# Kernel tuning notes

Hardware: AMD Instinct MI355X
Metric: run time of the kernel (lower is better)

Reference implementation:

```python
import jax, jax.numpy as jnp
import numpy as np

B, N, NODE_DIM = 64, 64, 192
H = 256          # node_hidden_dim
PDIM = 64        # property_embedding_dim
NUM_EDGE_TYPE = 5
T = 4            # message-passing rounds
E = 16384        # total edges (flattened batched graph)
E_SEL = 65536    # selected candidate pairs


def setup_inputs() -> dict:
    key = jax.random.key(0)
    ks = jax.random.split(key, 24)
    def g(k, shape, scale=0.05):
        return jax.random.normal(k, shape, dtype=jnp.float32) * scale
    inp = {
        "x": jax.random.normal(ks[0], (B, N, NODE_DIM), dtype=jnp.float32),
        "edge_index": jax.random.randint(ks[1], (2, E), 0, B * N, dtype=jnp.int32),
        "edge_attr": jax.random.uniform(ks[2], (E, NUM_EDGE_TYPE), dtype=jnp.float32),
        "props": jax.random.normal(ks[3], (B, 1), dtype=jnp.float32),
        "sel_b": jax.random.randint(ks[4], (E_SEL,), 0, B, dtype=jnp.int32),
        "sel_i": jax.random.randint(ks[5], (E_SEL,), 0, N, dtype=jnp.int32),
        "sel_j": jax.random.randint(ks[6], (E_SEL,), 0, N, dtype=jnp.int32),
        "golden_edge": jax.random.randint(ks[7], (E_SEL,), 0, NUM_EDGE_TYPE, dtype=jnp.int32),
        # parameters
        "W_prop": g(ks[8], (1, PDIM)), "b_prop": jnp.zeros((PDIM,), jnp.float32),
        "W_in": g(ks[9], (NODE_DIM, H)), "b_in": jnp.zeros((H,), jnp.float32),
        "W_msg": g(ks[10], (H + NUM_EDGE_TYPE, H)), "b_msg": jnp.zeros((H,), jnp.float32),
        "W_upd": g(ks[11], (2 * H, H)), "b_upd": jnp.zeros((H,), jnp.float32),
        "W_add": g(ks[12], (H + PDIM, H)), "b_add": jnp.zeros((H,), jnp.float32),
        "W1": g(ks[13], (2 * H, H)), "b1": jnp.zeros((H,), jnp.float32),
        "W2": g(ks[14], (H, H)), "b2": jnp.zeros((H,), jnp.float32),
        "W3": g(ks[15], (H, 2 * H)), "b3": jnp.zeros((2 * H,), jnp.float32),
        "W_out": g(ks[16], (2 * H, NUM_EDGE_TYPE)), "b_out": jnp.zeros((NUM_EDGE_TYPE,), jnp.float32),
    }
    return inp


def reference(x, edge_index, edge_attr, props, sel_b, sel_i, sel_j, golden_edge,
              W_prop, b_prop, W_in, b_in, W_msg, b_msg, W_upd, b_upd,
              W_add, b_add, W1, b1, W2, b2, W3, b3, W_out, b_out):
    BN = B * N
    node_x = x.reshape(BN, NODE_DIM)
    src, dst = edge_index[0], edge_index[1]

    # --- GNN node embedding (t rounds of message passing, opaque Encoder.embed_node) ---
    h = jax.nn.relu(node_x @ W_in + b_in)                       # [BN, H]
    for _ in range(T):
        msg_in = jnp.concatenate([h[src], edge_attr], axis=-1)  # [E, H+num_edge_type]
        msg = jax.nn.relu(msg_in @ W_msg + b_msg)               # [E, H]
        agg = jax.ops.segment_sum(msg, dst, num_segments=BN)    # [BN, H]
        h = jax.nn.relu(jnp.concatenate([h, agg], axis=-1) @ W_upd + b_upd)

    node_emb = h.reshape(B, N, H)

    # --- property conditioning + addition linear ---
    prop = props @ W_prop + b_prop                               # [B, PDIM]
    propp = jnp.broadcast_to(prop[:, None, :], (B, N, PDIM))
    node_embg = jnp.concatenate([node_emb, propp], axis=-1) @ W_add + b_add  # [B, N, H]

    # --- gather selected (src, dst) pairs directly (equiv. to repeat_interleave + boolean mask) ---
    flat = node_embg.reshape(BN, H)
    src_e = flat[sel_b * N + sel_i]                              # [E_SEL, H]
    dst_e = flat[sel_b * N + sel_j]                              # [E_SEL, H]
    pair = jnp.concatenate([src_e, dst_e], axis=-1)              # [E_SEL, 2H]

    # --- edge predictor MLP (3 layers, ReLU between) + output linear ---
    h1 = jax.nn.relu(pair @ W1 + b1)
    h2 = jax.nn.relu(h1 @ W2 + b2)
    h3 = h2 @ W3 + b3
    logits = h3 @ W_out + b_out                                  # [E_SEL, num_edge_type]

    # --- cross entropy (mean) ---
    logp = jax.nn.log_softmax(logits, axis=-1)
    loss = -jnp.mean(jnp.take_along_axis(logp, golden_edge[:, None].astype(jnp.int32), axis=-1))
    return loss
```

## Files before the change

### kernel.cpp

```cpp
#include <hip/hip_runtime.h>
#include <math.h>

#define BN 4096
#define N_PER_B 64
#define NE 16384
#define NSEL 65536
#define NET 5
#define PD 64
#define H1STR 260
#define FSTR 264
#define PTILES 2

typedef float f32x4 __attribute__((ext_vector_type(4)));
typedef float f32x16 __attribute__((ext_vector_type(16)));
typedef short short8 __attribute__((ext_vector_type(8)));
typedef short short4v __attribute__((ext_vector_type(4)));

__device__ __forceinline__ unsigned short f2bf(float f) {
    unsigned int u = __builtin_bit_cast(unsigned int, f);
    u += 0x7fff + ((u >> 16) & 1);
    return (unsigned short)(u >> 16);
}
__device__ __forceinline__ float bf_lo(unsigned int u) {
    return __builtin_bit_cast(float, u << 16);
}
__device__ __forceinline__ float bf_hi(unsigned int u) {
    return __builtin_bit_cast(float, u & 0xffff0000u);
}
__device__ __forceinline__ unsigned int pack2(float a, float b) {
    return (unsigned)f2bf(a) | ((unsigned)f2bf(b) << 16);
}
__device__ __forceinline__ short8 ld_frag(const unsigned short* p) {
    const short4v lo = *(const short4v*)(p);
    const short4v hi = *(const short4v*)(p + 4);
    return __builtin_shufflevector(lo, hi, 0, 1, 2, 3, 4, 5, 6, 7);
}
__device__ __forceinline__ unsigned int addrelu2(unsigned int a, unsigned int b, unsigned int c) {
    const float lo = fmaxf(bf_lo(a) + bf_lo(b) + bf_lo(c), 0.f);
    const float hi = fmaxf(bf_hi(a) + bf_hi(b) + bf_hi(c), 0.f);
    return pack2(lo, hi);
}

__global__ __launch_bounds__(256) void k_hist(const int* __restrict__ eidx,
                                              int* __restrict__ deg)
{
    const int e = blockIdx.x * 256 + threadIdx.x;
    atomicAdd(&deg[eidx[NE + e]], 1);
}

__global__ __launch_bounds__(256) void csr_scan(const int* __restrict__ deg,
                                                int* __restrict__ row_start,
                                                int* __restrict__ cursor)
{
    __shared__ int sums[256];
    const int tid = threadIdx.x;
    const int base = tid * 16;
    int local[16];
    int s = 0;
    #pragma unroll
    for (int i = 0; i < 16; ++i) { local[i] = s; s += deg[base + i]; }
    sums[tid] = s;
    __syncthreads();
    for (int off = 1; off < 256; off <<= 1) {
        const int v = sums[tid];
        const int add = (tid >= off) ? sums[tid - off] : 0;
        __syncthreads();
        sums[tid] = v + add;
        __syncthreads();
    }
    const int offset = (tid == 0) ? 0 : sums[tid - 1];
    #pragma unroll
    for (int i = 0; i < 16; ++i) {
        const int v = offset + local[i];
        row_start[base + i] = v;
        cursor[base + i] = v;
    }
    if (tid == 255) row_start[4096] = NE;
}

__global__ __launch_bounds__(256) void csr_scatter(const int* __restrict__ eidx,
                                                   int* __restrict__ cursor,
                                                   int* __restrict__ srcs)
{
    const int e = blockIdx.x * 256 + threadIdx.x;
    const int pos = atomicAdd(&cursor[eidx[NE + e]], 1);
    srcs[pos] = eidx[e] | (e << 12);
}

__global__ __launch_bounds__(256) void k_pre(
    const float* __restrict__ W_in, const float* __restrict__ W_msg,
    const float* __restrict__ W_upd, const float* __restrict__ W_add,
    const float* __restrict__ W1, const float* __restrict__ W2,
    const float* __restrict__ W3, const float* __restrict__ b3,
    const float* __restrict__ W_out, const float* __restrict__ b_out,
    const float* __restrict__ props, const float* __restrict__ W_prop,
    const float* __restrict__ b_prop, const float* __restrict__ b_add,
    const float* __restrict__ b_msg, const float* __restrict__ eattr,
    unsigned short* __restrict__ wbf, unsigned short* __restrict__ WfT,
    float* __restrict__ bfv, float* __restrict__ prop_add,
    unsigned short* __restrict__ ETc, float* __restrict__ out,
    int* __restrict__ deg)
{
    __shared__ __align__(16) char smem[16704];
    const int blk = blockIdx.x;
    const int tid = threadIdx.x;

    if (blk < 16) deg[blk * 256 + tid] = 0;
    if (blk == 0 && tid == 0) out[0] = 0.f;

    if (blk < 128) {
        float (*s)[65] = (float(*)[65])smem;
        const int wsel = blk >> 4;
        const int sub = blk & 15;
        const float* src; unsigned short* dst; int K = 256;
        switch (wsel) {
            case 0: src = W_in;              dst = wbf;                         K = 192; break;
            case 1: src = W_msg;             dst = wbf + 49152;                 break;
            case 2: src = W_upd;             dst = wbf + 49152 + 65536;         break;
            case 3: src = W_upd + 256 * 256; dst = wbf + 49152 + 2 * 65536;     break;
            case 4: src = W_add;             dst = wbf + 49152 + 3 * 65536;     break;
            case 5: src = W1;                dst = wbf + 49152 + 4 * 65536;     break;
            case 6: src = W1 + 256 * 256;    dst = wbf + 49152 + 5 * 65536;     break;
            default: src = W2;               dst = wbf + 49152 + 6 * 65536;     break;
        }
        const int k0 = (sub >> 2) * 64;
        const int n0 = (sub & 3) * 64;
        if (k0 >= K) return;
        const int tn = tid & 63;
        const int tg = tid >> 6;
        #pragma unroll
        for (int i = 0; i < 16; ++i) {
            const int kk = tg * 16 + i;
            s[kk][tn] = src[(size_t)(k0 + kk) * 256 + n0 + tn];
        }
        __syncthreads();
        #pragma unroll
        for (int i = 0; i < 16; ++i) {
            const int nn = tg * 16 + i;
            dst[(size_t)(n0 + nn) * K + k0 + tn] = f2bf(s[tn][nn]);
        }
    } else if (blk < 192) {
        const int b = blk - 128;
        const float pv = props[b];
        float acc = b_add[tid];
        for (int p = 0; p < PD; ++p) {
            const float e = fmaf(pv, W_prop[p], b_prop[p]);
            acc = fmaf(e, W_add[(256 + p) * 256 + tid], acc);
        }
        prop_add[b * 256 + tid] = acc;
    } else if (blk < 449) {
        float* part = (float*)smem;
        const int cb = blk - 192;
        float acc[NET] = {0.f, 0.f, 0.f, 0.f, 0.f};
        #pragma unroll
        for (int rep = 0; rep < 2; ++rep) {
            const int j = rep * 256 + tid;
            const float wv = (cb < 256) ? W3[(size_t)cb * 512 + j] : b3[j];
            #pragma unroll
            for (int t = 0; t < NET; ++t) acc[t] = fmaf(wv, W_out[j * NET + t], acc[t]);
        }
        #pragma unroll
        for (int t = 0; t < NET; ++t)
            for (int off = 32; off >= 1; off >>= 1) acc[t] += __shfl_down(acc[t], off);
        if ((tid & 63) == 0) {
            #pragma unroll
            for (int t = 0; t < NET; ++t) part[(tid >> 6) * NET + t] = acc[t];
        }
        __syncthreads();
        if (tid == 0) {
            float s[NET];
            #pragma unroll
            for (int t = 0; t < NET; ++t)
                s[t] = part[t] + part[NET + t] + part[2 * NET + t] + part[3 * NET + t];
            if (cb < 256) {
                #pragma unroll
                for (int t = 0; t < NET; ++t) WfT[t * 256 + cb] = f2bf(s[t]);
                #pragma unroll
                for (int t = NET; t < 16; ++t) WfT[t * 256 + cb] = 0;
            } else {
                #pragma unroll
                for (int t = 0; t < NET; ++t) bfv[t] = s[t] + b_out[t];
            }
        }
    } else {
        float* ea = (float*)smem;
        const int eb = (blk - 449) * 128;
        if (tid < 160)
            *(float4*)&ea[tid * 4] = *(const float4*)(eattr + (size_t)eb * 5 + tid * 4);
        __syncthreads();
        const float* Wme = W_msg + 256 * 256;
        const float w0 = Wme[0 * 256 + tid];
        const float w1 = Wme[1 * 256 + tid];
        const float w2 = Wme[2 * 256 + tid];
        const float w3 = Wme[3 * 256 + tid];
        const float w4 = Wme[4 * 256 + tid];
        const float bm = b_msg[tid];
        for (int i = 0; i < 128; ++i) {
            const float* a = ea + i * 5;
            float v = bm;
            v = fmaf(a[0], w0, v); v = fmaf(a[1], w1, v); v = fmaf(a[2], w2, v);
            v = fmaf(a[3], w3, v); v = fmaf(a[4], w4, v);
            ETc[(size_t)(eb + i) * 256 + tid] = f2bf(v);
        }
    }
}

__global__ __launch_bounds__(1024) void fstep(
    const float* __restrict__ x, const unsigned short* __restrict__ hbuf,
    const unsigned short* __restrict__ Pin, const unsigned short* __restrict__ ETc,
    const int* __restrict__ row_start, const int* __restrict__ srcs,
    const unsigned short* __restrict__ WaT, const unsigned short* __restrict__ WbT,
    const float* __restrict__ bias1,
    const unsigned short* __restrict__ Wp2T, const float* __restrict__ prop_add,
    const unsigned short* __restrict__ W1aT, const unsigned short* __restrict__ W1bT,
    unsigned short* __restrict__ hout, unsigned short* __restrict__ out1,
    unsigned short* __restrict__ out2, int mode)
{
    __shared__ __align__(16) unsigned short Hg[16 * FSTR];
    __shared__ __align__(16) unsigned short Ag[16 * FSTR];
    __shared__ __align__(16) unsigned short Hs[16 * FSTR];
    __shared__ __align__(16) unsigned short H2s[16 * FSTR];
    const int tid = threadIdx.x;
    const int w = tid >> 6;
    const int lane = tid & 63;
    const int q = lane >> 4;
    const int tx = lane & 15;
    const int m0 = blockIdx.x * 16;
    const int col = w * 16 + tx;

    if (mode != 0) {
        {
            const int r = tid >> 6;
            const int c4 = (tid & 63) * 4;
            *(uint2*)&Hg[r * FSTR + c4] =
                *(const uint2*)(hbuf + (size_t)(m0 + r) * 256 + c4);
        }
        {
            const int node = m0 + w;
            const int beg = row_start[node];
            const int end = row_start[node + 1];
            const int c = lane * 4;
            float a0 = 0.f, a1 = 0.f, a2 = 0.f, a3 = 0.f;
            int idx = beg;
            for (; idx + 3 < end; idx += 4) {
                const int k0 = srcs[idx],     k1 = srcs[idx + 1];
                const int k2 = srcs[idx + 2], k3 = srcs[idx + 3];
                const uint2 p0 = *(const uint2*)(Pin + (size_t)(k0 & 4095) * 256 + c);
                const uint2 p1 = *(const uint2*)(Pin + (size_t)(k1 & 4095) * 256 + c);
                const uint2 p2 = *(const uint2*)(Pin + (size_t)(k2 & 4095) * 256 + c);
                const uint2 p3 = *(const uint2*)(Pin + (size_t)(k3 & 4095) * 256 + c);
                const uint2 e0 = *(const uint2*)(ETc + (size_t)(k0 >> 12) * 256 + c);
                const uint2 e1 = *(const uint2*)(ETc + (size_t)(k1 >> 12) * 256 + c);
                const uint2 e2 = *(const uint2*)(ETc + (size_t)(k2 >> 12) * 256 + c);
                const uint2 e3 = *(const uint2*)(ETc + (size_t)(k3 >> 12) * 256 + c);
                a0 += fmaxf(bf_lo(p0.x) + bf_lo(e0.x), 0.f) + fmaxf(bf_lo(p1.x) + bf_lo(e1.x), 0.f)
                    + fmaxf(bf_lo(p2.x) + bf_lo(e2.x), 0.f) + fmaxf(bf_lo(p3.x) + bf_lo(e3.x), 0.f);
                a1 += fmaxf(bf_hi(p0.x) + bf_hi(e0.x), 0.f) + fmaxf(bf_hi(p1.x) + bf_hi(e1.x), 0.f)
                    + fmaxf(bf_hi(p2.x) + bf_hi(e2.x), 0.f) + fmaxf(bf_hi(p3.x) + bf_hi(e3.x), 0.f);
                a2 += fmaxf(bf_lo(p0.y) + bf_lo(e0.y), 0.f) + fmaxf(bf_lo(p1.y) + bf_lo(e1.y), 0.f)
                    + fmaxf(bf_lo(p2.y) + bf_lo(e2.y), 0.f) + fmaxf(bf_lo(p3.y) + bf_lo(e3.y), 0.f);
                a3 += fmaxf(bf_hi(p0.y) + bf_hi(e0.y), 0.f) + fmaxf(bf_hi(p1.y) + bf_hi(e1.y), 0.f)
                    + fmaxf(bf_hi(p2.y) + bf_hi(e2.y), 0.f) + fmaxf(bf_hi(p3.y) + bf_hi(e3.y), 0.f);
            }
            for (; idx < end; ++idx) {
                const int pk = srcs[idx];
                const uint2 pu = *(const uint2*)(Pin + (size_t)(pk & 4095) * 256 + c);
                const uint2 eu = *(const uint2*)(ETc + (size_t)(pk >> 12) * 256 + c);
                a0 += fmaxf(bf_lo(pu.x) + bf_lo(eu.x), 0.f);
                a1 += fmaxf(bf_hi(pu.x) + bf_hi(eu.x), 0.f);
                a2 += fmaxf(bf_lo(pu.y) + bf_lo(eu.y), 0.f);
                a3 += fmaxf(bf_hi(pu.y) + bf_hi(eu.y), 0.f);
            }
            uint2 o; o.x = pack2(a0, a1); o.y = pack2(a2, a3);
            *(uint2*)&Ag[w * FSTR + c] = o;
        }
        __syncthreads();
    }

    f32x4 acc = (f32x4)0.f;
    if (mode == 0) {
        #pragma unroll
        for (int s = 0; s < 6; ++s) {
            const int k0 = s * 32;
            const float* ap = x + (size_t)(m0 + tx) * 192 + k0 + q * 8;
            const float4 v0 = *(const float4*)ap;
            const float4 v1 = *(const float4*)(ap + 4);
            short8 af;
            af[0] = (short)f2bf(v0.x); af[1] = (short)f2bf(v0.y);
            af[2] = (short)f2bf(v0.z); af[3] = (short)f2bf(v0.w);
            af[4] = (short)f2bf(v1.x); af[5] = (short)f2bf(v1.y);
            af[6] = (short)f2bf(v1.z); af[7] = (short)f2bf(v1.w);
            const short8 bfr = *(const short8*)(WaT + (size_t)col * 192 + k0 + q * 8);
            acc = __builtin_amdgcn_mfma_f32_16x16x32_bf16(af, bfr, acc, 0, 0, 0);
        }
    } else {
        #pragma unroll
        for (int s = 0; s < 8; ++s) {
            const int k0 = s * 32;
            const short8 af = *(const short8*)&Hg[tx * FSTR + k0 + q * 8];
            const short8 bfr = *(const short8*)(WaT + (size_t)col * 256 + k0 + q * 8);
            acc = __builtin_amdgcn_mfma_f32_16x16x32_bf16(af, bfr, acc, 0, 0, 0);
        }
        #pragma unroll
        for (int s = 0; s < 8; ++s) {
            const int k0 = s * 32;
            const short8 af = *(const short8*)&Ag[tx * FSTR + k0 + q * 8];
            const short8 bfr = *(const short8*)(WbT + (size_t)col * 256 + k0 + q * 8);
            acc = __builtin_amdgcn_mfma_f32_16x16x32_bf16(af, bfr, acc, 0, 0, 0);
        }
    }
    {
        const float bv = bias1[col];
        #pragma unroll
        for (int r = 0; r < 4; ++r) {
            const int row = q * 4 + r;
            const unsigned short us = f2bf(fmaxf(acc[r] + bv, 0.f));
            Hs[row * FSTR + col] = us;
            if (mode < 2) hout[(size_t)(m0 + row) * 256 + col] = us;
        }
    }
    __syncthreads();

    acc = (f32x4)0.f;
    #pragma unroll
    for (int s = 0; s < 8; ++s) {
        const int k0 = s * 32;
        const short8 af = *(const short8*)&Hs[tx * FSTR + k0 + q * 8];
        const short8 bfr = *(const short8*)(Wp2T + (size_t)col * 256 + k0 + q * 8);
        acc = __builtin_amdgcn_mfma_f32_16x16x32_bf16(af, bfr, acc, 0, 0, 0);
    }
    if (mode < 2) {
        #pragma unroll
        for (int r = 0; r < 4; ++r)
            out1[(size_t)(m0 + q * 4 + r) * 256 + col] = f2bf(acc[r]);
        return;
    }
    {
        const float pv = prop_add[(m0 >> 6) * 256 + col];
        #pragma unroll
        for (int r = 0; r < 4; ++r)
            H2s[(q * 4 + r) * FSTR + col] = f2bf(acc[r] + pv);
    }
    __syncthreads();

    for (int which = 0; which < 2; ++which) {
        const unsigned short* WT = which ? W1bT : W1aT;
        unsigned short* op = which ? out2 : out1;
        acc = (f32x4)0.f;
        #pragma unroll
        for (int s = 0; s < 8; ++s) {
            const int k0 = s * 32;
            const short8 af = *(const short8*)&H2s[tx * FSTR + k0 + q * 8];
            const short8 bfr = *(const short8*)(WT + (size_t)col * 256 + k0 + q * 8);
            acc = __builtin_amdgcn_mfma_f32_16x16x32_bf16(af, bfr, acc, 0, 0, 0);
        }
        #pragma unroll
        for (int r = 0; r < 4; ++r)
            op[(size_t)(m0 + q * 4 + r) * 256 + col] = f2bf(acc[r]);
    }
}

__global__ __launch_bounds__(512, 2) void pair_k(
    const unsigned short* __restrict__ A1t, const unsigned short* __restrict__ A2t,
    const float* __restrict__ b1, const unsigned short* __restrict__ W2T,
    const float* __restrict__ b2, const unsigned short* __restrict__ WfT,
    const float* __restrict__ bfv,
    const int* __restrict__ sel_b, const int* __restrict__ sel_i,
    const int* __restrict__ sel_j, const int* __restrict__ golden,
    float* __restrict__ out)
{
    __shared__ __align__(16) unsigned short sbuf[64 * H1STR];
    __shared__ __align__(16) unsigned short b1s[256];
    __shared__ float Lg[64 * 8];
    __shared__ int sidx[64 * PTILES], didx[64 * PTILES], gold[64 * PTILES];

    const int tid = threadIdx.x;
    const int w = tid >> 6;
    const int lane = tid & 63;
    const int q = lane >> 4;
    const int tx = lane & 15;
    const int m = lane & 31;
    const int hh = lane >> 5;
    const int e0 = blockIdx.x * 64 * PTILES;

    if (tid < 64 * PTILES) {
        const int e = e0 + tid;
        const int b = sel_b[e];
        sidx[tid] = b * N_PER_B + sel_i[e];
        didx[tid] = b * N_PER_B + sel_j[e];
        gold[tid] = golden[e];
    }
    if (tid < 256) b1s[tid] = f2bf(b1[tid]);

    short8 Breg[16];
    {
        const unsigned short* bb = W2T + (size_t)(w * 32 + m) * 256 + hh * 8;
        #pragma unroll
        for (int s = 0; s < 16; ++s)
            Breg[s] = *(const short8*)(bb + s * 16);
    }
    __syncthreads();

    float total = 0.f;

    for (int t = 0; t < PTILES; ++t) {
        {
            const int hw = tid >> 5;
            #pragma unroll
            for (int j = 0; j < 4; ++j) {
                const int p = j * 16 + hw;
                const unsigned short* r1 = A1t + (size_t)sidx[t * 64 + p] * 256 + m * 8;
                const unsigned short* r2 = A2t + (size_t)didx[t * 64 + p] * 256 + m * 8;
                const uint4 u1 = *(const uint4*)r1;
                const uint4 u2 = *(const uint4*)r2;
                const uint4 ub = *(const uint4*)(b1s + m * 8);
                uint2 lo2, hi2;
                lo2.x = addrelu2(u1.x, u2.x, ub.x);
                lo2.y = addrelu2(u1.y, u2.y, ub.y);
                hi2.x = addrelu2(u1.z, u2.z, ub.z);
                hi2.y = addrelu2(u1.w, u2.w, ub.w);
                unsigned short* dbase = sbuf + p * H1STR + m * 8;
                *(uint2*)(dbase) = lo2;
                *(uint2*)(dbase + 4) = hi2;
            }
        }
        __syncthreads();

        f32x16 acc0 = (f32x16)0.f;
        f32x16 acc1 = (f32x16)0.f;
        {
            const unsigned short* a0row = sbuf + (size_t)m * H1STR + hh * 8;
            const unsigned short* a1row = a0row + 32 * H1STR;
            #pragma unroll
            for (int s = 0; s < 16; ++s) {
                const short8 af0 = ld_frag(a0row + s * 16);
                acc0 = __builtin_amdgcn_mfma_f32_32x32x16_bf16(af0, Breg[s], acc0, 0, 0, 0);
                const short8 af1 = ld_frag(a1row + s * 16);
                acc1 = __builtin_amdgcn_mfma_f32_32x32x16_bf16(af1, Breg[s], acc1, 0, 0, 0);
            }
        }
        __syncthreads();

        {
            const int col = w * 32 + m;
            const float bv = b2[col];
            #pragma unroll
            for (int reg = 0; reg < 16; ++reg) {
                const int prow = (reg & 3) + 8 * (reg >> 2) + 4 * hh;
                sbuf[prow * H1STR + col] = f2bf(fmaxf(acc0[reg] + bv, 0.f));
                sbuf[(32 + prow) * H1STR + col] = f2bf(fmaxf(acc1[reg] + bv, 0.f));
            }
        }
        __syncthreads();

        if (w < 4) {
            f32x4 accL = (f32x4)0.f;
            const unsigned short* a2row = sbuf + (size_t)(w * 16 + tx) * H1STR + q * 8;
            const unsigned short* bWf = WfT + (size_t)tx * 256 + q * 8;
            #pragma unroll
            for (int s = 0; s < 8; ++s) {
                const short8 af = ld_frag(a2row + s * 32);
                const short8 bfr = *(const short8*)(bWf + s * 32);
                accL = __builtin_amdgcn_mfma_f32_16x16x32_bf16(af, bfr, accL, 0, 0, 0);
            }
            if (tx < NET) {
                const float bb = bfv[tx];
                #pragma unroll
                for (int reg = 0; reg < 4; ++reg)
                    Lg[(w * 16 + q * 4 + reg) * 8 + tx] = accL[reg] + bb;
            }
        }
        __syncthreads();

        if (tid < 64) {
            float lg[NET];
            #pragma unroll
            for (int tt = 0; tt < NET; ++tt) lg[tt] = Lg[tid * 8 + tt];
            float mx = lg[0];
            #pragma unroll
            for (int tt = 1; tt < NET; ++tt) mx = fmaxf(mx, lg[tt]);
            float s = 0.f;
            #pragma unroll
            for (int tt = 0; tt < NET; ++tt) s += expf(lg[tt] - mx);
            float ls = mx + logf(s) - lg[gold[t * 64 + tid]];
            #pragma unroll
            for (int off = 32; off >= 1; off >>= 1) ls += __shfl_xor(ls, off);
            total += ls;
        }
        __syncthreads();
    }

    if (tid == 0) atomicAdd(out, total * (1.0f / NSEL));
}

extern "C" void kernel_launch(void* const* d_in, const int* in_sizes, int n_in,
                              void* d_out, int out_size, void* d_ws, size_t ws_size,
                              hipStream_t stream) {
    (void)in_sizes; (void)n_in; (void)out_size; (void)ws_size;
    const float* x      = (const float*)d_in[0];
    const int*   eidx   = (const int*)d_in[1];
    const float* eattr  = (const float*)d_in[2];
    const float* props  = (const float*)d_in[3];
    const int*   sel_b  = (const int*)d_in[4];
    const int*   sel_i  = (const int*)d_in[5];
    const int*   sel_j  = (const int*)d_in[6];
    const int*   golden = (const int*)d_in[7];
    const float* W_prop = (const float*)d_in[8];
    const float* b_prop = (const float*)d_in[9];
    const float* W_in   = (const float*)d_in[10];
    const float* b_in   = (const float*)d_in[11];
    const float* W_msg  = (const float*)d_in[12];
    const float* b_msg  = (const float*)d_in[13];
    const float* W_upd  = (const float*)d_in[14];
    const float* b_upd  = (const float*)d_in[15];
    const float* W_add  = (const float*)d_in[16];
    const float* b_add  = (const float*)d_in[17];
    const float* W1     = (const float*)d_in[18];
    const float* b1     = (const float*)d_in[19];
    const float* W2     = (const float*)d_in[20];
    const float* b2     = (const float*)d_in[21];
    const float* W3     = (const float*)d_in[22];
    const float* b3     = (const float*)d_in[23];
    const float* W_out  = (const float*)d_in[24];
    const float* b_out  = (const float*)d_in[25];

    const size_t SEG = (size_t)BN * 256;
    unsigned short* P0   = (unsigned short*)d_ws;
    unsigned short* P1   = P0 + SEG;
    unsigned short* hA   = P1 + SEG;
    unsigned short* hB   = hA + SEG;
    unsigned short* ETc  = hB + SEG;
    unsigned short* wbf  = ETc + (size_t)NE * 256;
    unsigned short* W_inT  = wbf;
    unsigned short* WmT    = wbf + 49152;
    unsigned short* WuaT   = WmT + 65536;
    unsigned short* WubT   = WuaT + 65536;
    unsigned short* W_addT = WubT + 65536;
    unsigned short* W1aT   = W_addT + 65536;
    unsigned short* W1bT   = W1aT + 65536;
    unsigned short* W2T    = W1bT + 65536;
    unsigned short* WfT    = W2T + 65536;
    float* prop_add = (float*)(WfT + 4096);
    float* bfv = prop_add + 64 * 256;
    int* row_start = (int*)(bfv + 16);
    int* srcs      = row_start + 4104;
    int* deg       = srcs + NE;
    int* cursor    = deg + 4096;

    k_pre<<<577, 256, 0, stream>>>(W_in, W_msg, W_upd, W_add, W1, W2, W3, b3,
                                   W_out, b_out, props, W_prop, b_prop, b_add,
                                   b_msg, eattr, wbf, WfT, bfv, prop_add,
                                   ETc, (float*)d_out, deg);
    k_hist<<<NE / 256, 256, 0, stream>>>(eidx, deg);
    csr_scan<<<1, 256, 0, stream>>>(deg, row_start, cursor);
    csr_scatter<<<NE / 256, 256, 0, stream>>>(eidx, cursor, srcs);

    fstep<<<256, 1024, 0, stream>>>(x, nullptr, nullptr, ETc, row_start, srcs,
                                    W_inT, nullptr, b_in, WmT, nullptr, nullptr, nullptr,
                                    hA, P0, nullptr, 0);
    fstep<<<256, 1024, 0, stream>>>(nullptr, hA, P0, ETc, row_start, srcs,
                                    WuaT, WubT, b_upd, WmT, nullptr, nullptr, nullptr,
                                    hB, P1, nullptr, 1);
    fstep<<<256, 1024, 0, stream>>>(nullptr, hB, P1, ETc, row_start, srcs,
                                    WuaT, WubT, b_upd, WmT, nullptr, nullptr, nullptr,
                                    hA, P0, nullptr, 1);
    fstep<<<256, 1024, 0, stream>>>(nullptr, hA, P0, ETc, row_start, srcs,
                                    WuaT, WubT, b_upd, WmT, nullptr, nullptr, nullptr,
                                    hB, P1, nullptr, 1);
    fstep<<<256, 1024, 0, stream>>>(nullptr, hB, P1, ETc, row_start, srcs,
                                    WuaT, WubT, b_upd, W_addT, prop_add, W1aT, W1bT,
                                    nullptr, P0, hA, 2);

    pair_k<<<NSEL / (64 * PTILES), 512, 0, stream>>>(P0, hA, b1, W2T, b2, WfT, bfv,
                                    sel_b, sel_i, sel_j, golden, (float*)d_out);
}
```

Measured before the change: 245.0 us.

## Fold CSR scan and scatter into first fstep launch via extra blocks

The histogram kernel now also records each edge's rank within its destination bucket. The separate scan and scatter kernels are removed. Their work moves into 64 extra blocks of the mode-0 fstep launch: each block redoes the 4096-entry prefix scan in shared memory and scatters its slice of edges. This cuts two kernel launches and their serialization, at the cost of redundant scans across blocks. Mode-0 fstep does not read the CSR, so running both in one launch is safe.

```diff
diff --git a/kernel.cpp b/kernel.cpp
--- a/kernel.cpp
+++ b/kernel.cpp
@@ -41,50 +41,12 @@
     return pack2(lo, hi);
 }
 
-__global__ __launch_bounds__(256) void k_hist(const int* __restrict__ eidx,
-                                              int* __restrict__ deg)
+__global__ __launch_bounds__(256) void khist_rank(const int* __restrict__ eidx,
+                                                  int* __restrict__ deg,
+                                                  int* __restrict__ rank)
 {
     const int e = blockIdx.x * 256 + threadIdx.x;
-    atomicAdd(&deg[eidx[NE + e]], 1);
-}
-
-__global__ __launch_bounds__(256) void csr_scan(const int* __restrict__ deg,
-                                                int* __restrict__ row_start,
-                                                int* __restrict__ cursor)
-{
-    __shared__ int sums[256];
-    const int tid = threadIdx.x;
-    const int base = tid * 16;
-    int local[16];
-    int s = 0;
-    #pragma unroll
-    for (int i = 0; i < 16; ++i) { local[i] = s; s += deg[base + i]; }
-    sums[tid] = s;
-    __syncthreads();
-    for (int off = 1; off < 256; off <<= 1) {
-        const int v = sums[tid];
-        const int add = (tid >= off) ? sums[tid - off] : 0;
-        __syncthreads();
-        sums[tid] = v + add;
-        __syncthreads();
-    }
-    const int offset = (tid == 0) ? 0 : sums[tid - 1];
-    #pragma unroll
-    for (int i = 0; i < 16; ++i) {
-        const int v = offset + local[i];
-        row_start[base + i] = v;
-        cursor[base + i] = v;
-    }
-    if (tid == 255) row_start[4096] = NE;
-}
-
-__global__ __launch_bounds__(256) void csr_scatter(const int* __restrict__ eidx,
-                                                   int* __restrict__ cursor,
-                                                   int* __restrict__ srcs)
-{
-    const int e = blockIdx.x * 256 + threadIdx.x;
-    const int pos = atomicAdd(&cursor[eidx[NE + e]], 1);
-    srcs[pos] = eidx[e] | (e << 12);
+    rank[e] = atomicAdd(&deg[eidx[NE + e]], 1);
 }
 
 __global__ __launch_bounds__(256) void k_pre(
@@ -214,13 +176,50 @@
     const unsigned short* __restrict__ Wp2T, const float* __restrict__ prop_add,
     const unsigned short* __restrict__ W1aT, const unsigned short* __restrict__ W1bT,
     unsigned short* __restrict__ hout, unsigned short* __restrict__ out1,
-    unsigned short* __restrict__ out2, int mode)
+    unsigned short* __restrict__ out2, int mode,
+    const int* __restrict__ eidx, const int* __restrict__ deg,
+    const int* __restrict__ rank, int* __restrict__ srcs_w,
+    int* __restrict__ row_start_w)
 {
-    __shared__ __align__(16) unsigned short Hg[16 * FSTR];
-    __shared__ __align__(16) unsigned short Ag[16 * FSTR];
-    __shared__ __align__(16) unsigned short Hs[16 * FSTR];
-    __shared__ __align__(16) unsigned short H2s[16 * FSTR];
+    __shared__ __align__(16) char smemb[4 * 16 * FSTR * 2];
+    unsigned short* Hg  = (unsigned short*)(smemb);
+    unsigned short* Ag  = (unsigned short*)(smemb + 8448);
+    unsigned short* Hs  = (unsigned short*)(smemb + 16896);
+    unsigned short* H2s = (unsigned short*)(smemb + 25344);
     const int tid = threadIdx.x;
+
+    if (mode == 0 && blockIdx.x >= 256) {
+        int* sdeg = (int*)smemb;
+        int* ssum = (int*)(smemb + 16384);
+        const int t4 = tid * 4;
+        const int4 v = *(const int4*)(deg + t4);
+        const int l1 = v.x, l2 = v.x + v.y, l3 = v.x + v.y + v.z;
+        ssum[tid] = l3 + v.w;
+        __syncthreads();
+        for (int off = 1; off < 1024; off <<= 1) {
+            const int vv = ssum[tid];
+            const int add = (tid >= off) ? ssum[tid - off] : 0;
+            __syncthreads();
+            ssum[tid] = vv + add;
+            __syncthreads();
+        }
+        const int offset = (tid == 0) ? 0 : ssum[tid - 1];
+        int4 rs;
+        rs.x = offset; rs.y = offset + l1; rs.z = offset + l2; rs.w = offset + l3;
+        *(int4*)(sdeg + t4) = rs;
+        if (blockIdx.x == 256) {
+            *(int4*)(row_start_w + t4) = rs;
+            if (tid == 1023) row_start_w[4096] = NE;
+        }
+        __syncthreads();
+        if (tid < 256) {
+            const int e = (blockIdx.x - 256) * 256 + tid;
+            const int d = eidx[NE + e];
+            srcs_w[sdeg[d] + rank[e]] = eidx[e] | (e << 12);
+        }
+        return;
+    }
+
     const int w = tid >> 6;
     const int lane = tid & 63;
     const int q = lane >> 4;
@@ -232,7 +231,7 @@
         {
             const int r = tid >> 6;
             const int c4 = (tid & 63) * 4;
-            *(uint2*)&Hg[r * FSTR + c4] =
+            *(uint2*)(Hg + r * FSTR + c4) =
                 *(const uint2*)(hbuf + (size_t)(m0 + r) * 256 + c4);
         }
         {
@@ -272,7 +271,7 @@
                 a3 += fmaxf(bf_hi(pu.y) + bf_hi(eu.y), 0.f);
             }
             uint2 o; o.x = pack2(a0, a1); o.y = pack2(a2, a3);
-            *(uint2*)&Ag[w * FSTR + c] = o;
+            *(uint2*)(Ag + w * FSTR + c) = o;
         }
         __syncthreads();
     }
@@ -297,14 +296,14 @@
         #pragma unroll
         for (int s = 0; s < 8; ++s) {
             const int k0 = s * 32;
-            const short8 af = *(const short8*)&Hg[tx * FSTR + k0 + q * 8];
+            const short8 af = *(const short8*)(Hg + tx * FSTR + k0 + q * 8);
             const short8 bfr = *(const short8*)(WaT + (size_t)col * 256 + k0 + q * 8);
             acc = __builtin_amdgcn_mfma_f32_16x16x32_bf16(af, bfr, acc, 0, 0, 0);
         }
         #pragma unroll
         for (int s = 0; s < 8; ++s) {
             const int k0 = s * 32;
-            const short8 af = *(const short8*)&Ag[tx * FSTR + k0 + q * 8];
+            const short8 af = *(const short8*)(Ag + tx * FSTR + k0 + q * 8);
             const short8 bfr = *(const short8*)(WbT + (size_t)col * 256 + k0 + q * 8);
             acc = __builtin_amdgcn_mfma_f32_16x16x32_bf16(af, bfr, acc, 0, 0, 0);
         }
@@ -325,7 +324,7 @@
     #pragma unroll
     for (int s = 0; s < 8; ++s) {
         const int k0 = s * 32;
-        const short8 af = *(const short8*)&Hs[tx * FSTR + k0 + q * 8];
+        const short8 af = *(const short8*)(Hs + tx * FSTR + k0 + q * 8);
         const short8 bfr = *(const short8*)(Wp2T + (size_t)col * 256 + k0 + q * 8);
         acc = __builtin_amdgcn_mfma_f32_16x16x32_bf16(af, bfr, acc, 0, 0, 0);
     }
@@ -350,7 +349,7 @@
         #pragma unroll
         for (int s = 0; s < 8; ++s) {
             const int k0 = s * 32;
-            const short8 af = *(const short8*)&H2s[tx * FSTR + k0 + q * 8];
+            const short8 af = *(const short8*)(H2s + tx * FSTR + k0 + q * 8);
             const short8 bfr = *(const short8*)(WT + (size_t)col * 256 + k0 + q * 8);
             acc = __builtin_amdgcn_mfma_f32_16x16x32_bf16(af, bfr, acc, 0, 0, 0);
         }
@@ -545,31 +544,34 @@
     int* row_start = (int*)(bfv + 16);
     int* srcs      = row_start + 4104;
     int* deg       = srcs + NE;
-    int* cursor    = deg + 4096;
+    int* rank      = deg + 4096;
 
     k_pre<<<577, 256, 0, stream>>>(W_in, W_msg, W_upd, W_add, W1, W2, W3, b3,
                                    W_out, b_out, props, W_prop, b_prop, b_add,
                                    b_msg, eattr, wbf, WfT, bfv, prop_add,
                                    ETc, (float*)d_out, deg);
-    k_hist<<<NE / 256, 256, 0, stream>>>(eidx, deg);
-    csr_scan<<<1, 256, 0, stream>>>(deg, row_start, cursor);
-    csr_scatter<<<NE / 256, 256, 0, stream>>>(eidx, cursor, srcs);
-
-    fstep<<<256, 1024, 0, stream>>>(x, nullptr, nullptr, ETc, row_start, srcs,
+    khist_rank<<<NE / 256, 256, 0, stream>>>(eidx, deg, rank);
+
+    fstep<<<320, 1024, 0, stream>>>(x, nullptr, nullptr, ETc, row_start, srcs,
                                     W_inT, nullptr, b_in, WmT, nullptr, nullptr, nullptr,
-                                    hA, P0, nullptr, 0);
+                                    hA, P0, nullptr, 0,
+                                    eidx, deg, rank, srcs, row_start);
     fstep<<<256, 1024, 0, stream>>>(nullptr, hA, P0, ETc, row_start, srcs,
                                     WuaT, WubT, b_upd, WmT, nullptr, nullptr, nullptr,
-                                    hB, P1, nullptr, 1);
+                                    hB, P1, nullptr, 1,
+                                    nullptr, nullptr, nullptr, nullptr, nullptr);
     fstep<<<256, 1024, 0, stream>>>(nullptr, hB, P1, ETc, row_start, srcs,
                                     WuaT, WubT, b_upd, WmT, nullptr, nullptr, nullptr,
-                                    hA, P0, nullptr, 1);
+                                    hA, P0, nullptr, 1,
+                                    nullptr, nullptr, nullptr, nullptr, nullptr);
     fstep<<<256, 1024, 0, stream>>>(nullptr, hA, P0, ETc, row_start, srcs,
                                     WuaT, WubT, b_upd, WmT, nullptr, nullptr, nullptr,
-                                    hB, P1, nullptr, 1);
+                                    hB, P1, nullptr, 1,
+                                    nullptr, nullptr, nullptr, nullptr, nullptr);
     fstep<<<256, 1024, 0, stream>>>(nullptr, hB, P1, ETc, row_start, srcs,
                                     WuaT, WubT, b_upd, W_addT, prop_add, W1aT, W1bT,
-                                    nullptr, P0, hA, 2);
+                                    nullptr, P0, hA, 2,
+                                    nullptr, nullptr, nullptr, nullptr, nullptr);
 
     pair_k<<<NSEL / (64 * PTILES), 512, 0, stream>>>(P0, hA, b1, W2T, b2, WfT, bfv,
                                     sel_b, sel_i, sel_j, golden, (float*)d_out);
```

Result: no change. 242.4 us (-1.1%).
